# Optimization experiments

Measured on AMD Instinct MI355X. Metric: run time of the kernel, lower is better.

## Reference

```python
import math
import jax, jax.numpy as jnp
import numpy as np

B, S, H = 2, 2048, 1024
NH = 16
HD = H // NH            # 64
ROT = int(HD * 0.25)    # 16
QKV_SLOTS = 1024
PROJ_SLOTS = 1024
FFN_SLOTS = 4096
EPS = 1e-5


def gelu_l2_norm(x, axis=-1):
    # F.gelu (exact erf) then L2-normalize and rescale by sqrt(dim)
    g = jax.nn.gelu(x, approximate=False)
    n = jnp.linalg.norm(g, ord=2, axis=axis, keepdims=True)
    return g / n * math.sqrt(g.shape[axis])


def layer_norm(x, w, b):
    mu = jnp.mean(x, axis=-1, keepdims=True)
    var = jnp.mean(jnp.square(x - mu), axis=-1, keepdims=True)
    return (x - mu) * jax.lax.rsqrt(var + EPS) * w + b


def pattention(x, key_tok, val_tok):
    # [.., in] @ [slots, in]^T -> [.., slots]; NOTE: scale MULTIPLIES (as in source)
    aw = jnp.einsum('bsh,ph->bsp', x, key_tok) * math.sqrt(x.shape[-1])
    aw = gelu_l2_norm(aw, axis=-1)
    return jnp.einsum('bsp,pd->bsd', aw, val_tok)


def rotary_cos_sin(seq_len, rot_dim, base=10000.0):
    inv_freq = 1.0 / (base ** (jnp.arange(0, rot_dim, 2, dtype=jnp.float32) / rot_dim))
    t = jnp.arange(seq_len, dtype=jnp.float32)
    freqs = jnp.einsum('s,d->sd', t, inv_freq)           # [S, rot/2]
    emb = jnp.concatenate([freqs, freqs], axis=-1)       # [S, rot]
    return jnp.cos(emb), jnp.sin(emb)


def rotate_half(x):
    x1, x2 = jnp.split(x, 2, axis=-1)
    return jnp.concatenate([-x2, x1], axis=-1)


def setup_inputs() -> dict:
    key = jax.random.key(0)
    ks = jax.random.split(key, 12)
    p = lambda k, shape: jax.random.normal(k, shape, dtype=jnp.float32) * 0.02
    return {
        'x': jax.random.normal(ks[0], (B, S, H), dtype=jnp.float32),
        'ln1_w': jnp.ones((H,), jnp.float32), 'ln1_b': jnp.zeros((H,), jnp.float32),
        'ln2_w': jnp.ones((H,), jnp.float32), 'ln2_b': jnp.zeros((H,), jnp.float32),
        'q_key': p(ks[1], (QKV_SLOTS, H)), 'q_val': p(ks[2], (QKV_SLOTS, H)),
        'k_key': p(ks[3], (QKV_SLOTS, H)), 'k_val': p(ks[4], (QKV_SLOTS, H)),
        'v_key': p(ks[5], (QKV_SLOTS, H)), 'v_val': p(ks[6], (QKV_SLOTS, H)),
        'proj_key': p(ks[7], (PROJ_SLOTS, H)), 'proj_val': p(ks[8], (PROJ_SLOTS, H)),
        'ffn_key': p(ks[9], (FFN_SLOTS, H)), 'ffn_val': p(ks[10], (FFN_SLOTS, H)),
    }


def reference(x, ln1_w, ln1_b, ln2_w, ln2_b, q_key, q_val, k_key, k_val,
              v_key, v_val, proj_key, proj_val, ffn_key, ffn_val):
    residual = x
    xn = layer_norm(x, ln1_w, ln1_b)
    q = pattention(xn, q_key, q_val).reshape(B, S, NH, HD)
    k = pattention(xn, k_key, k_val).reshape(B, S, NH, HD)
    v = pattention(xn, v_key, v_val).reshape(B, S, NH, HD)

    cos, sin = rotary_cos_sin(S, ROT)          # [S, ROT]
    cos = cos[None, :, None, :]
    sin = sin[None, :, None, :]
    q_rot, q_pass = q[..., :ROT], q[..., ROT:]
    k_rot, k_pass = k[..., :ROT], k[..., ROT:]
    q_rot = q_rot * cos + rotate_half(q_rot) * sin
    k_rot = k_rot * cos + rotate_half(k_rot) * sin
    q = jnp.concatenate([q_rot, q_pass], axis=-1).transpose(0, 2, 1, 3)  # [B,NH,S,HD]
    k = jnp.concatenate([k_rot, k_pass], axis=-1).transpose(0, 2, 1, 3)
    v = v.transpose(0, 2, 1, 3)

    scale = math.sqrt(HD)
    causal = jnp.triu(jnp.ones((S, S), dtype=bool), k=1)
    attn_mask = jnp.where(causal, jnp.float32(-10000.0), jnp.float32(0.0))
    aw = jnp.einsum('bhqd,bhkd->bhqk', q, k) / scale + attn_mask
    aw = gelu_l2_norm(aw, axis=-1)
    o = jnp.einsum('bhqk,bhkd->bhqd', aw, v)
    o = o.transpose(0, 2, 1, 3).reshape(B, S, H)

    x = residual + pattention(o, proj_key, proj_val)
    residual = x
    x = residual + pattention(layer_norm(x, ln2_w, ln2_b), ffn_key, ffn_val)
    return x
```

## Files before the change

kernel.cpp:

```cpp
#include <hip/hip_runtime.h>

typedef __bf16 bf16x8 __attribute__((ext_vector_type(8)));
typedef float f32x4 __attribute__((ext_vector_type(4)));
typedef unsigned short u16;

__device__ __forceinline__ float b2f(u16 u) {
  union { unsigned int i; float f; } v; v.i = ((unsigned int)u) << 16; return v.f;
}
__device__ __forceinline__ u16 f2b(float f) {
  union { float f; unsigned int i; } v; v.f = f;
  unsigned int x = v.i;
  x += 0x7fffu + ((x >> 16) & 1u);
  return (u16)(x >> 16);
}
__device__ __forceinline__ float gelu_f(float x) {
  float x2 = x * x;
  float p = x * (1.5957691216f + 0.0713548162f * x2);
  float e = __expf(p);
  float r = __builtin_amdgcn_rcpf(1.0f + e);
  return x - x * r;
}
__device__ __forceinline__ void async16(const u16* g, u16* l) {
  __builtin_amdgcn_global_load_lds(
      (const __attribute__((address_space(1))) void*)g,
      (__attribute__((address_space(3))) void*)l, 16, 0, 0);
}
__device__ __forceinline__ void swz(int& bn, int& bm, int& bz) {
  int gx = (int)gridDim.x, gy = (int)gridDim.y;
  int flat = (int)(blockIdx.x + gridDim.x * (blockIdx.y + gridDim.y * blockIdx.z));
  int seq = flat >> 3;
  int nbm = gy >> 3;
  bm = (flat & 7) * nbm + seq % nbm;
  int rest = seq / nbm;
  bn = rest % gx;
  bz = rest / gx;
}

union U4 { uint4 u; u16 s[8]; };

__global__ __launch_bounds__(256) void prep_kernel(
    const float* __restrict__ qk, const float* __restrict__ kk,
    const float* __restrict__ vk, const float* __restrict__ pk,
    const float* __restrict__ fk, u16* __restrict__ w, float* __restrict__ ssqz,
    const float* __restrict__ qv, const float* __restrict__ kv,
    const float* __restrict__ vv, const float* __restrict__ pv,
    const float* __restrict__ fv, u16* __restrict__ valsT, u16* __restrict__ fvT,
    const float* __restrict__ x, const float* __restrict__ lnw,
    const float* __restrict__ lnb, u16* __restrict__ xn) {
  __shared__ float t[32][33];
  int id = (int)blockIdx.x;
  int tid = threadIdx.x;
  if (id < 9216) {
    int z = id >> 10;
    int i = (id & 1023) * 256 + tid;
    if (z == 8) {
      if (i < 20480) ssqz[i] = 0.f;
      return;
    }
    const float* in = (z == 0) ? qk : (z == 1) ? kk : (z == 2) ? vk : (z == 3) ? pk
                      : fk + (size_t)(z - 4) * 1048576;
    u16* o = w + (size_t)z * 1048576;
    float4 f = ((const float4*)in)[i];
    ushort4 s;
    s.x = f2b(f.x); s.y = f2b(f.y); s.z = f2b(f.z); s.w = f2b(f.w);
    ((ushort4*)o)[i] = s;
  } else if (id < 17408) {
    int rid = id - 9216;
    int bc = rid & 31, br = (rid >> 5) & 31, z = rid >> 10;
    const float* in; u16* o; int Rout, rowoff;
    if (z < 4) {
      in = (z == 0) ? qv : (z == 1) ? kv : (z == 2) ? vv : pv;
      o = valsT + (size_t)z * 1048576; Rout = 1024; rowoff = 0;
    } else {
      in = fv + (size_t)(z - 4) * 1048576;
      o = fvT; Rout = 4096; rowoff = (z - 4) * 1024;
    }
    int r = tid >> 5, cc = tid & 31;
    #pragma unroll
    for (int i = 0; i < 4; ++i)
      t[r + i * 8][cc] = in[(size_t)(br * 32 + r + i * 8) * 1024 + bc * 32 + cc];
    __syncthreads();
    #pragma unroll
    for (int i = 0; i < 4; ++i)
      o[(size_t)(bc * 32 + r + i * 8) * Rout + rowoff + br * 32 + cc] = f2b(t[cc][r + i * 8]);
  } else {
    int wv = tid >> 6, lane = tid & 63;
    int row = (id - 17408) * 4 + wv;
    const float* xr = x + (size_t)row * 1024;
    float4 v[4];
    float s = 0.f, s2 = 0.f;
    #pragma unroll
    for (int i = 0; i < 4; ++i) {
      v[i] = ((const float4*)xr)[lane + 64 * i];
      s += v[i].x + v[i].y + v[i].z + v[i].w;
      s2 += v[i].x * v[i].x + v[i].y * v[i].y + v[i].z * v[i].z + v[i].w * v[i].w;
    }
    #pragma unroll
    for (int m = 1; m < 64; m <<= 1) { s += __shfl_xor(s, m); s2 += __shfl_xor(s2, m); }
    float mu = s * (1.0f / 1024.0f);
    float inv = rsqrtf(s2 * (1.0f / 1024.0f) - mu * mu + 1e-5f);
    u16* orow = xn + (size_t)row * 1024;
    #pragma unroll
    for (int i = 0; i < 4; ++i) {
      int c = (lane + 64 * i) * 4;
      ushort4 o;
      o.x = f2b((v[i].x - mu) * inv * lnw[c]     + lnb[c]);
      o.y = f2b((v[i].y - mu) * inv * lnw[c + 1] + lnb[c + 1]);
      o.z = f2b((v[i].z - mu) * inv * lnw[c + 2] + lnb[c + 2]);
      o.w = f2b((v[i].w - mu) * inv * lnw[c + 3] + lnb[c + 3]);
      ((ushort4*)orow)[lane + 64 * i] = o;
    }
  }
}

__global__ __launch_bounds__(256) void ln_kernel(const float* __restrict__ x,
    const float* __restrict__ w, const float* __restrict__ b, u16* __restrict__ out) {
  int wv = threadIdx.x >> 6, lane = threadIdx.x & 63;
  int row = blockIdx.x * 4 + wv;
  const float* xr = x + (size_t)row * 1024;
  float4 v[4];
  float s = 0.f, s2 = 0.f;
  #pragma unroll
  for (int i = 0; i < 4; ++i) {
    v[i] = ((const float4*)xr)[lane + 64 * i];
    s += v[i].x + v[i].y + v[i].z + v[i].w;
    s2 += v[i].x * v[i].x + v[i].y * v[i].y + v[i].z * v[i].z + v[i].w * v[i].w;
  }
  #pragma unroll
  for (int m = 1; m < 64; m <<= 1) { s += __shfl_xor(s, m); s2 += __shfl_xor(s2, m); }
  float mu = s * (1.0f / 1024.0f);
  float inv = rsqrtf(s2 * (1.0f / 1024.0f) - mu * mu + 1e-5f);
  u16* orow = out + (size_t)row * 1024;
  #pragma unroll
  for (int i = 0; i < 4; ++i) {
    int c = (lane + 64 * i) * 4;
    ushort4 o;
    o.x = f2b((v[i].x - mu) * inv * w[c]     + b[c]);
    o.y = f2b((v[i].y - mu) * inv * w[c + 1] + b[c + 1]);
    o.z = f2b((v[i].z - mu) * inv * w[c + 2] + b[c + 2]);
    o.w = f2b((v[i].w - mu) * inv * w[c + 3] + b[c + 3]);
    ((ushort4*)orow)[lane + 64 * i] = o;
  }
}


template <int TM>
__global__ __launch_bounds__(256) void gemm_key(
    const u16* __restrict__ A, size_t sAz,
    const u16* __restrict__ B, size_t sBz,
    u16* __restrict__ C, size_t sCz,
    float* __restrict__ ssqb, size_t sSz,
    int N, int K, float alpha) {
  constexpr int AI = TM / 32;
  constexpr int G = TM / 64 + 2;
  __shared__ __align__(16) u16 As[3][TM * 32];
  __shared__ __align__(16) u16 Bs[3][128 * 32];
  int bn, bm, bz;
  swz(bn, bm, bz);
  const u16* Ab = A + (size_t)bz * sAz + (size_t)bm * TM * K;
  const u16* Bb = B + (size_t)bz * sBz + (size_t)bn * 128 * K;
  int tid = threadIdx.x, lane = tid & 63, wv = tid >> 6;
  int quad = lane >> 4, l16 = lane & 15;
  int lr = lane >> 2;
  int lcs = ((lane & 3) ^ ((lane >> 3) & 3)) * 8;
  int rq = quad ^ ((l16 >> 1) & 3);
  int wm = wv >> 1, wn = wv & 1;
  int RB = wm * (TM / 2), CB = wn * 64;
  auto STAGE = [&](int k0, int buf) {
    #pragma unroll
    for (int t = 0; t < TM / 64; ++t) {
      int ia = wv * (TM / 64) + t;
      async16(Ab + (size_t)(ia * 16 + lr) * K + k0 + lcs, &As[buf][ia * 512]);
    }
    #pragma unroll
    for (int t = 0; t < 2; ++t) {
      int ib = wv * 2 + t;
      async16(Bb + (size_t)(ib * 16 + lr) * K + k0 + lcs, &Bs[buf][ib * 512]);
    }
  };
  f32x4 zero = {0.f, 0.f, 0.f, 0.f};
  f32x4 acc[AI][4];
  #pragma unroll
  for (int i = 0; i < AI; ++i)
    #pragma unroll
    for (int j = 0; j < 4; ++j) acc[i][j] = zero;
  int NT = K >> 5;
  STAGE(0, 0);
  STAGE(32, 1);
  int cur = 0;
  for (int t = 0; t < NT; ++t) {
    if (t + 1 < NT) asm volatile("s_waitcnt vmcnt(%0)" :: "i"(G) : "memory");
    else            asm volatile("s_waitcnt vmcnt(0)" ::: "memory");
    __builtin_amdgcn_s_barrier();
    __builtin_amdgcn_sched_barrier(0);
    bf16x8 af[AI], bf[4];
    #pragma unroll
    for (int i = 0; i < AI; ++i)
      af[i] = *(const bf16x8*)&As[cur][(RB + i * 16 + l16) * 32 + rq * 8];
    #pragma unroll
    for (int j = 0; j < 4; ++j)
      bf[j] = *(const bf16x8*)&Bs[cur][(CB + j * 16 + l16) * 32 + rq * 8];
    if (t + 2 < NT) {
      int nb = cur + 2; if (nb >= 3) nb -= 3;
      STAGE((t + 2) * 32, nb);
    }
    #pragma unroll
    for (int i = 0; i < AI; ++i)
      #pragma unroll
      for (int j = 0; j < 4; ++j)
        acc[i][j] = __builtin_amdgcn_mfma_f32_16x16x32_bf16(af[i], bf[j], acc[i][j], 0, 0, 0);
    cur = (cur == 2) ? 0 : cur + 1;
  }
  #pragma unroll
  for (int i = 0; i < AI; ++i) {
    int rbase = bm * TM + RB + i * 16 + quad * 4;
    float srow[4] = {0.f, 0.f, 0.f, 0.f};
    #pragma unroll
    for (int j = 0; j < 4; ++j) {
      int c = bn * 128 + CB + j * 16 + l16;
      #pragma unroll
      for (int reg = 0; reg < 4; ++reg) {
        float g = gelu_f(acc[i][j][reg] * alpha);
        srow[reg] += g * g;
        C[(size_t)bz * sCz + (size_t)(rbase + reg) * N + c] = f2b(g);
      }
    }
    #pragma unroll
    for (int reg = 0; reg < 4; ++reg) {
      float s = srow[reg];
      s += __shfl_xor(s, 1); s += __shfl_xor(s, 2);
      s += __shfl_xor(s, 4); s += __shfl_xor(s, 8);
      if (l16 == 0) atomicAdd(&ssqb[bz * sSz + rbase + reg], s);
    }
  }
}

__global__ __launch_bounds__(256, 2) void gemm_fkey(
    const u16* __restrict__ A,
    const u16* __restrict__ B,
    u16* __restrict__ C,
    float* __restrict__ ssqb,
    int N, int K, float alpha) {
  __shared__ __align__(16) u16 As[2][128 * 32];
  __shared__ __align__(16) u16 Bs[3][256 * 32];
  int bn, bm, bz;
  swz(bn, bm, bz);
  const u16* Ab = A + (size_t)bm * 128 * K;
  const u16* Bb = B + (size_t)bn * 256 * K;
  int tid = threadIdx.x, lane = tid & 63, wv = tid >> 6;
  int quad = lane >> 4, l16 = lane & 15;
  int lr = lane >> 2;
  int lcs = ((lane & 3) ^ ((lane >> 3) & 3)) * 8;
  int rq = quad ^ ((l16 >> 1) & 3);
  int wm = wv >> 1, wn = wv & 1;
  int RB = wm * 64, CB = wn * 128;
  auto STAGE_A = [&](int k0, int buf) {
    #pragma unroll
    for (int t = 0; t < 2; ++t) {
      int ia = wv * 2 + t;
      async16(Ab + (size_t)(ia * 16 + lr) * K + k0 + lcs, &As[buf][ia * 512]);
    }
  };
  auto STAGE_B = [&](int k0, int buf) {
    #pragma unroll
    for (int t = 0; t < 4; ++t) {
      int ib = wv * 4 + t;
      async16(Bb + (size_t)(ib * 16 + lr) * K + k0 + lcs, &Bs[buf][ib * 512]);
    }
  };
  f32x4 zero = {0.f, 0.f, 0.f, 0.f};
  f32x4 acc[4][8];
  #pragma unroll
  for (int i = 0; i < 4; ++i)
    #pragma unroll
    for (int j = 0; j < 8; ++j) acc[i][j] = zero;
  int NT = K >> 5;
  STAGE_A(0, 0);
  STAGE_B(0, 0);
  STAGE_B(32, 1);
  int cb = 0;
  for (int t = 0; t < NT; ++t) {
    if (t + 1 < NT) asm volatile("s_waitcnt vmcnt(4)" ::: "memory");
    else            asm volatile("s_waitcnt vmcnt(0)" ::: "memory");
    __builtin_amdgcn_s_barrier();
    __builtin_amdgcn_sched_barrier(0);
    bf16x8 af[4], bf[8];
    #pragma unroll
    for (int i = 0; i < 4; ++i)
      af[i] = *(const bf16x8*)&As[t & 1][(RB + i * 16 + l16) * 32 + rq * 8];
    #pragma unroll
    for (int j = 0; j < 8; ++j)
      bf[j] = *(const bf16x8*)&Bs[cb][(CB + j * 16 + l16) * 32 + rq * 8];
    if (t + 1 < NT) STAGE_A((t + 1) * 32, (t + 1) & 1);
    if (t + 2 < NT) {
      int nb = cb + 2; if (nb >= 3) nb -= 3;
      STAGE_B((t + 2) * 32, nb);
    }
    #pragma unroll
    for (int i = 0; i < 4; ++i)
      #pragma unroll
      for (int j = 0; j < 8; ++j)
        acc[i][j] = __builtin_amdgcn_mfma_f32_16x16x32_bf16(af[i], bf[j], acc[i][j], 0, 0, 0);
    cb = (cb == 2) ? 0 : cb + 1;
  }
  #pragma unroll
  for (int i = 0; i < 4; ++i) {
    int rbase = bm * 128 + RB + i * 16 + quad * 4;
    float srow[4] = {0.f, 0.f, 0.f, 0.f};
    #pragma unroll
    for (int j = 0; j < 8; ++j) {
      int c = bn * 256 + CB + j * 16 + l16;
      #pragma unroll
      for (int reg = 0; reg < 4; ++reg) {
        float g = gelu_f(acc[i][j][reg] * alpha);
        srow[reg] += g * g;
        C[(size_t)(rbase + reg) * N + c] = f2b(g);
      }
    }
    #pragma unroll
    for (int reg = 0; reg < 4; ++reg) {
      float s = srow[reg];
      s += __shfl_xor(s, 1); s += __shfl_xor(s, 2);
      s += __shfl_xor(s, 4); s += __shfl_xor(s, 8);
      if (l16 == 0) atomicAdd(&ssqb[rbase + reg], s);
    }
  }
}

template <int TM, int MODE, bool ROT>
__global__ __launch_bounds__(256) void gemm_val(
    const u16* __restrict__ A, size_t sAz,
    const u16* __restrict__ B, size_t sBz,
    void* __restrict__ C, size_t sCz,
    const float* __restrict__ ssqb, size_t sSz,
    int N, int K, int kzs, int klen, float sqrtP, const float* __restrict__ res) {
  constexpr int AI = TM / 32;
  constexpr int G = TM / 64 + 2;
  __shared__ __align__(16) u16 As[3][TM * 32];
  __shared__ __align__(16) u16 Bs[3][128 * 32];
  int bn, bm, bz;
  swz(bn, bm, bz);
  const u16* Ab = A + (size_t)bz * sAz + (size_t)bm * TM * K;
  const u16* Bb = B + (size_t)bz * sBz + (size_t)bn * 128 * K;
  int tid = threadIdx.x, lane = tid & 63, wv = tid >> 6;
  int quad = lane >> 4, l16 = lane & 15;
  int lr = lane >> 2;
  int lcs = ((lane & 3) ^ ((lane >> 3) & 3)) * 8;
  int rq = quad ^ ((l16 >> 1) & 3);
  int wm = wv >> 1, wn = wv & 1;
  int RB = wm * (TM / 2), CB = wn * 64;
  int kb0 = bz * kzs;
  auto STAGE = [&](int k0, int buf) {
    #pragma unroll
    for (int t = 0; t < TM / 64; ++t) {
      int ia = wv * (TM / 64) + t;
      async16(Ab + (size_t)(ia * 16 + lr) * K + kb0 + k0 + lcs, &As[buf][ia * 512]);
    }
    #pragma unroll
    for (int t = 0; t < 2; ++t) {
      int ib = wv * 2 + t;
      async16(Bb + (size_t)(ib * 16 + lr) * K + kb0 + k0 + lcs, &Bs[buf][ib * 512]);
    }
  };
  f32x4 zero = {0.f, 0.f, 0.f, 0.f};
  f32x4 acc[AI][4];
  #pragma unroll
  for (int i = 0; i < AI; ++i)
    #pragma unroll
    for (int j = 0; j < 4; ++j) acc[i][j] = zero;
  int NT = klen >> 5;
  STAGE(0, 0);
  STAGE(32, 1);
  int cur = 0;
  for (int t = 0; t < NT; ++t) {
    if (t + 1 < NT) asm volatile("s_waitcnt vmcnt(%0)" :: "i"(G) : "memory");
    else            asm volatile("s_waitcnt vmcnt(0)" ::: "memory");
    __builtin_amdgcn_s_barrier();
    __builtin_amdgcn_sched_barrier(0);
    bf16x8 af[AI], bf[4];
    #pragma unroll
    for (int i = 0; i < AI; ++i)
      af[i] = *(const bf16x8*)&As[cur][(RB + i * 16 + l16) * 32 + rq * 8];
    #pragma unroll
    for (int j = 0; j < 4; ++j)
      bf[j] = *(const bf16x8*)&Bs[cur][(CB + j * 16 + l16) * 32 + rq * 8];
    if (t + 2 < NT) {
      int nb = cur + 2; if (nb >= 3) nb -= 3;
      STAGE((t + 2) * 32, nb);
    }
    #pragma unroll
    for (int i = 0; i < AI; ++i)
      #pragma unroll
      for (int j = 0; j < 4; ++j)
        acc[i][j] = __builtin_amdgcn_mfma_f32_16x16x32_bf16(af[i], bf[j], acc[i][j], 0, 0, 0);
    cur = (cur == 2) ? 0 : cur + 1;
  }
  #pragma unroll
  for (int i = 0; i < AI; ++i) {
    int rbase = bm * TM + RB + i * 16 + quad * 4;
    float sc[4];
    if (MODE < 2) {
      #pragma unroll
      for (int reg = 0; reg < 4; ++reg)
        sc[reg] = sqrtP * rsqrtf(ssqb[bz * sSz + rbase + reg]);
    }
    #pragma unroll
    for (int j = 0; j < 4; ++j) {
      int c = bn * 128 + CB + j * 16 + l16;
      #pragma unroll
      for (int reg = 0; reg < 4; ++reg) {
        float v = acc[i][j][reg];
        size_t idx = (size_t)(rbase + reg) * N + c;
        if (MODE == 0) {
          float vs = v * sc[reg];
          if (ROT && j == 0) {
            float prt = __shfl_xor(vs, 8);
            if (bz < 2) {
              int seq = (rbase + reg) & 2047;
              float fr = exp2f((float)(l16 & 7) * -1.66096404744368f);
              float ang = (float)seq * fr;
              float c_ = __cosf(ang), s_ = __sinf(ang);
              vs = (l16 < 8) ? (vs * c_ - prt * s_) : (vs * c_ + prt * s_);
            }
          }
          ((u16*)C)[(size_t)bz * sCz + idx] = f2b(vs);
        } else if (MODE == 1) {
          ((float*)C)[idx] = v * sc[reg] + res[idx];
        } else {
          ((float*)C)[(size_t)bz * sCz + idx] = v;
        }
      }
    }
  }
}

__global__ __launch_bounds__(256) void vt_kernel(const u16* __restrict__ vb,
                                                 u16* __restrict__ vT) {
  __shared__ __align__(16) u16 T[64][72];
  int st = blockIdx.x, bh = blockIdx.y;
  int b = bh >> 4, h = bh & 15;
  int tid = threadIdx.x;
  #pragma unroll
  for (int i = 0; i < 2; ++i) {
    int l = tid + 256 * i;
    int s = l >> 3, dc = l & 7;
    *(uint4*)&T[s][dc * 8] =
        *(const uint4*)(vb + (size_t)(b * 2048 + st * 64 + s) * 1024 + h * 64 + dc * 8);
  }
  __syncthreads();
  #pragma unroll
  for (int i = 0; i < 2; ++i) {
    int l = tid + 256 * i;
    int d = l >> 3, scid = l & 7;
    int blk = (scid >> 2) * 32;
    int qq = (scid & 3) * 4;
    U4 u;
    #pragma unroll
    for (int j = 0; j < 8; ++j)
      u.s[j] = T[blk + (j >> 2) * 16 + qq + (j & 3)][d];
    *(uint4*)(vT + ((size_t)bh * 64 + d) * 2048 + st * 64 + scid * 8) = u.u;
  }
}

__global__ __launch_bounds__(256) void attn_kernel(
    const u16* __restrict__ qb, const u16* __restrict__ kb,
    const u16* __restrict__ vT, u16* __restrict__ ob) {
  __shared__ __align__(16) u16 Qs[64 * 64];
  __shared__ __align__(16) u16 Ks[2][64 * 64];
  __shared__ __align__(16) u16 Vts[2][64 * 64];
  int bh = blockIdx.x;
  int qt = 31 - (int)blockIdx.y;
  int b = bh >> 4, h = bh & 15;
  const u16* qp = qb + (size_t)b * 2048 * 1024 + h * 64;
  const u16* kp = kb + (size_t)b * 2048 * 1024 + h * 64;
  const u16* vp = vT + (size_t)bh * 64 * 2048;
  int tid = threadIdx.x, lane = tid & 63, wv = tid >> 6;
  int quad = lane >> 4, l16 = lane & 15;
  int lr8 = lane >> 3;
  int lc8s = ((lane & 7) ^ lr8) * 8;
  int rx = (l16 & 7) << 3;
  int MR = wv * 16;
  int nkt = qt + 1;
  #pragma unroll
  for (int t = 0; t < 2; ++t) {
    int idx = wv * 2 + t;
    async16(qp + (size_t)(qt * 64 + idx * 8 + lr8) * 1024 + lc8s, &Qs[idx * 512]);
    async16(kp + (size_t)(idx * 8 + lr8) * 1024 + lc8s, &Ks[0][idx * 512]);
    async16(vp + (size_t)(idx * 8 + lr8) * 2048 + lc8s, &Vts[0][idx * 512]);
  }
  f32x4 zero = {0.f, 0.f, 0.f, 0.f};
  f32x4 oacc[4];
  #pragma unroll
  for (int dn = 0; dn < 4; ++dn) oacc[dn] = zero;
  float ssql = 0.f;
  bf16x8 bq0 = {}, bq1 = {};
  for (int kt = 0, cur = 0; kt < nkt; ++kt, cur ^= 1) {
    __syncthreads();
    if (kt == 0) {
      bq0 = *(const bf16x8*)&Qs[((MR + l16) * 64 + quad * 8) ^ rx];
      bq1 = *(const bf16x8*)&Qs[((MR + l16) * 64 + 32 + quad * 8) ^ rx];
    }
    if (kt + 1 < nkt) {
      #pragma unroll
      for (int t = 0; t < 2; ++t) {
        int idx = wv * 2 + t;
        async16(kp + (size_t)((kt + 1) * 64 + idx * 8 + lr8) * 1024 + lc8s, &Ks[cur ^ 1][idx * 512]);
        async16(vp + (size_t)(idx * 8 + lr8) * 2048 + (kt + 1) * 64 + lc8s, &Vts[cur ^ 1][idx * 512]);
      }
    }
    bool dg = (kt == qt);
    #pragma unroll
    for (int kc = 0; kc < 2; ++kc) {
      bf16x8 pf;
      #pragma unroll
      for (int snh = 0; snh < 2; ++snh) {
        int sn = kc * 2 + snh;
        bf16x8 ak0 = *(const bf16x8*)&Ks[cur][((sn * 16 + l16) * 64 + quad * 8) ^ rx];
        bf16x8 ak1 = *(const bf16x8*)&Ks[cur][((sn * 16 + l16) * 64 + 32 + quad * 8) ^ rx];
        f32x4 st = zero;
        st = __builtin_amdgcn_mfma_f32_16x16x32_bf16(ak0, bq0, st, 0, 0, 0);
        st = __builtin_amdgcn_mfma_f32_16x16x32_bf16(ak1, bq1, st, 0, 0, 0);
        #pragma unroll
        for (int r = 0; r < 4; ++r) {
          float gl = gelu_f(st[r] * 0.125f);
          if (dg && (sn * 16 + quad * 4 + r > MR + l16)) gl = 0.f;
          ssql += gl * gl;
          pf[snh * 4 + r] = (__bf16)gl;
        }
      }
      #pragma unroll
      for (int dn = 0; dn < 4; ++dn) {
        bf16x8 bv = *(const bf16x8*)&Vts[cur][((dn * 16 + l16) * 64 + kc * 32 + quad * 8) ^ rx];
        oacc[dn] = __builtin_amdgcn_mfma_f32_16x16x32_bf16(pf, bv, oacc[dn], 0, 0, 0);
      }
    }
  }
  ssql += __shfl_xor(ssql, 16);
  ssql += __shfl_xor(ssql, 32);
  float sc = 45.254834f * rsqrtf(ssql);
  #pragma unroll
  for (int dn = 0; dn < 4; ++dn)
    #pragma unroll
    for (int r = 0; r < 4; ++r) {
      float scr = __shfl(sc, quad * 4 + r);
      int row = qt * 64 + MR + quad * 4 + r;
      int col = h * 64 + dn * 16 + l16;
      ob[(size_t)(b * 2048 + row) * 1024 + col] = f2b(oacc[dn][r] * scr);
    }
}

__global__ __launch_bounds__(256) void fin_kernel(
    const float* __restrict__ p0, const float* __restrict__ p1,
    const float* __restrict__ x1, const float* __restrict__ ssqf,
    float* __restrict__ out) {
  int row = blockIdx.x, t = threadIdx.x;
  float s = 64.0f * rsqrtf(ssqf[row]);
  size_t base = (size_t)row * 1024 + t * 4;
  float4 a = *(const float4*)(p0 + base);
  float4 b = *(const float4*)(p1 + base);
  float4 r = *(const float4*)(x1 + base);
  float4 o;
  o.x = r.x + s * (a.x + b.x); o.y = r.y + s * (a.y + b.y);
  o.z = r.z + s * (a.z + b.z); o.w = r.w + s * (a.w + b.w);
  *(float4*)(out + base) = o;
}

extern "C" void kernel_launch(void* const* d_in, const int* in_sizes, int n_in,
                              void* d_out, int out_size, void* d_ws, size_t ws_size,
                              hipStream_t stream) {
  const float* x    = (const float*)d_in[0];
  const float* ln1w = (const float*)d_in[1];
  const float* ln1b = (const float*)d_in[2];
  const float* ln2w = (const float*)d_in[3];
  const float* ln2b = (const float*)d_in[4];
  const float* qk   = (const float*)d_in[5];
  const float* qv   = (const float*)d_in[6];
  const float* kk   = (const float*)d_in[7];
  const float* kv   = (const float*)d_in[8];
  const float* vk   = (const float*)d_in[9];
  const float* vv   = (const float*)d_in[10];
  const float* pk   = (const float*)d_in[11];
  const float* pv   = (const float*)d_in[12];
  const float* fk   = (const float*)d_in[13];
  const float* fv   = (const float*)d_in[14];
  float* out = (float*)d_out;

  const size_t M1 = 1048576;
  u16* w = (u16*)d_ws;
  u16* wkeys  = w;
  u16* wpk    = w + 3 * M1;
  u16* wfk    = w + 4 * M1;
  u16* wvalsT = w + 8 * M1;
  u16* wpvT   = w + 11 * M1;
  u16* wfvT   = w + 12 * M1;
  u16* xn     = w + 16 * M1;
  u16* gq     = w + 20 * M1;
  u16* ob     = w + 20 * M1;
  u16* vT     = w + 24 * M1;
  u16* gp     = w + 28 * M1;
  u16* gf     = w + 20 * M1;
  u16* qb     = w + 36 * M1;
  u16* kb     = w + 40 * M1;
  u16* vb     = w + 44 * M1;
  float* ssq_qkv  = (float*)(w + 48 * M1);
  float* ssq_proj = ssq_qkv + 12288;
  float* ssq_ffn  = ssq_qkv + 16384;
  float* x1 = (float*)(w + 52 * M1);
  float* p0 = (float*)w;
  float* p1 = (float*)(w + 36 * M1);

  dim3 blk(256);
  prep_kernel<<<18432, blk, 0, stream>>>(
      qk, kk, vk, pk, fk, w, ssq_qkv,
      qv, kv, vv, pv, fv, wvalsT, wfvT,
      x, ln1w, ln1b, xn);

  gemm_key<128><<<dim3(8, 32, 3), blk, 0, stream>>>(
      xn, 0, wkeys, M1, gq, 4 * M1, ssq_qkv, 4096, 1024, 1024, 32.0f);
  gemm_val<128, 0, true><<<dim3(8, 32, 3), blk, 0, stream>>>(
      gq, 4 * M1, wvalsT, M1, qb, 4 * M1, ssq_qkv, 4096, 1024, 1024, 0, 1024, 32.0f, nullptr);

  vt_kernel<<<dim3(32, 32), blk, 0, stream>>>(vb, vT);
  attn_kernel<<<dim3(32, 32), blk, 0, stream>>>(qb, kb, vT, ob);

  gemm_key<64><<<dim3(8, 64, 1), blk, 0, stream>>>(
      ob, 0, wpk, 0, gp, 0, ssq_proj, 0, 1024, 1024, 32.0f);
  gemm_val<64, 1, false><<<dim3(8, 64, 1), blk, 0, stream>>>(
      gp, 0, wpvT, 0, x1, 0, ssq_proj, 0, 1024, 1024, 0, 1024, 32.0f, x);

  ln_kernel<<<1024, blk, 0, stream>>>(x1, ln2w, ln2b, xn);
  gemm_fkey<<<dim3(16, 32, 1), blk, 0, stream>>>(
      xn, wfk, gf, ssq_ffn, 4096, 1024, 32.0f);
  gemm_val<128, 2, false><<<dim3(8, 32, 2), blk, 0, stream>>>(
      gf, 0, wfvT, 0, p0, 18 * M1, ssq_ffn, 0, 1024, 4096, 2048, 2048, 0.0f, nullptr);
  fin_kernel<<<4096, blk, 0, stream>>>(p0, p1, x1, ssq_ffn, out);
}
```

Baseline: 407.9 us.

## Split long causal attention rows into two KV halves with a combine kernel

The causal attention grid is rebalanced: query tiles 17..31 are each split into two blocks covering halves of the key range, and the two blocks write unnormalized partial outputs and partial sum-of-squares to scratch. A new combine kernel adds the partials, applies the L2 rescale and writes bf16 output. This aims to cut the tail from the longest query tiles on a 32x32 grid. It costs an extra launch and fp32 scratch traffic. GELU also switches to exp2 with pre-scaled coefficients.

Result: no change. 401.5 us (-1.6%).

```diff
diff --git a/kernel.cpp b/kernel.cpp
--- a/kernel.cpp
+++ b/kernel.cpp
@@ -15,8 +15,8 @@
 }
 __device__ __forceinline__ float gelu_f(float x) {
   float x2 = x * x;
-  float p = x * (1.5957691216f + 0.0713548162f * x2);
-  float e = __expf(p);
+  float p = x * (2.3022083f + 0.1029434f * x2);
+  float e = __builtin_amdgcn_exp2f(p);
   float r = __builtin_amdgcn_rcpf(1.0f + e);
   return x - x * r;
 }
@@ -142,7 +142,6 @@
     ((ushort4*)orow)[lane + 64 * i] = o;
   }
 }
-
 
 template <int TM>
 __global__ __launch_bounds__(256) void gemm_key(
@@ -463,16 +462,26 @@
 }
 
 __global__ __launch_bounds__(256) void attn_kernel(
-    const u16* __restrict__ qb, const u16* __restrict__ kb,
-    const u16* __restrict__ vT, u16* __restrict__ ob) {
+    const u16* __restrict__ qb, const u16* __restrict__ kbp,
+    const u16* __restrict__ vT, u16* __restrict__ ob,
+    float* __restrict__ pP, float* __restrict__ ssqP) {
   __shared__ __align__(16) u16 Qs[64 * 64];
   __shared__ __align__(16) u16 Ks[2][64 * 64];
   __shared__ __align__(16) u16 Vts[2][64 * 64];
   int bh = blockIdx.x;
-  int qt = 31 - (int)blockIdx.y;
-  int b = bh >> 4, h = bh & 15;
-  const u16* qp = qb + (size_t)b * 2048 * 1024 + h * 64;
-  const u16* kp = kb + (size_t)b * 2048 * 1024 + h * 64;
+  int y = (int)blockIdx.y;
+  int qt, kb, ke, half = 0;
+  bool part = false;
+  if (y == 0) { qt = 16; kb = 0; ke = 17; }
+  else if (y <= 30) {
+    int s = y - 1;
+    qt = 31 - (s >> 1); half = s & 1; part = true;
+    int n = qt + 1, h = (n + 1) >> 1;
+    kb = half ? h : 0; ke = half ? n : h;
+  } else { qt = 46 - y; kb = 0; ke = qt + 1; }
+  int b = bh >> 4, h16 = bh & 15;
+  const u16* qp = qb + (size_t)b * 2048 * 1024 + h16 * 64;
+  const u16* kp = kbp + (size_t)b * 2048 * 1024 + h16 * 64;
   const u16* vp = vT + (size_t)bh * 64 * 2048;
   int tid = threadIdx.x, lane = tid & 63, wv = tid >> 6;
   int quad = lane >> 4, l16 = lane & 15;
@@ -480,13 +489,12 @@
   int lc8s = ((lane & 7) ^ lr8) * 8;
   int rx = (l16 & 7) << 3;
   int MR = wv * 16;
-  int nkt = qt + 1;
   #pragma unroll
   for (int t = 0; t < 2; ++t) {
     int idx = wv * 2 + t;
     async16(qp + (size_t)(qt * 64 + idx * 8 + lr8) * 1024 + lc8s, &Qs[idx * 512]);
-    async16(kp + (size_t)(idx * 8 + lr8) * 1024 + lc8s, &Ks[0][idx * 512]);
-    async16(vp + (size_t)(idx * 8 + lr8) * 2048 + lc8s, &Vts[0][idx * 512]);
+    async16(kp + (size_t)(kb * 64 + idx * 8 + lr8) * 1024 + lc8s, &Ks[0][idx * 512]);
+    async16(vp + (size_t)(idx * 8 + lr8) * 2048 + kb * 64 + lc8s, &Vts[0][idx * 512]);
   }
   f32x4 zero = {0.f, 0.f, 0.f, 0.f};
   f32x4 oacc[4];
@@ -494,13 +502,13 @@
   for (int dn = 0; dn < 4; ++dn) oacc[dn] = zero;
   float ssql = 0.f;
   bf16x8 bq0 = {}, bq1 = {};
-  for (int kt = 0, cur = 0; kt < nkt; ++kt, cur ^= 1) {
+  for (int kt = kb, cur = 0; kt < ke; ++kt, cur ^= 1) {
     __syncthreads();
-    if (kt == 0) {
+    if (kt == kb) {
       bq0 = *(const bf16x8*)&Qs[((MR + l16) * 64 + quad * 8) ^ rx];
       bq1 = *(const bf16x8*)&Qs[((MR + l16) * 64 + 32 + quad * 8) ^ rx];
     }
-    if (kt + 1 < nkt) {
+    if (kt + 1 < ke) {
       #pragma unroll
       for (int t = 0; t < 2; ++t) {
         int idx = wv * 2 + t;
@@ -537,16 +545,50 @@
   }
   ssql += __shfl_xor(ssql, 16);
   ssql += __shfl_xor(ssql, 32);
-  float sc = 45.254834f * rsqrtf(ssql);
-  #pragma unroll
-  for (int dn = 0; dn < 4; ++dn)
-    #pragma unroll
-    for (int r = 0; r < 4; ++r) {
-      float scr = __shfl(sc, quad * 4 + r);
-      int row = qt * 64 + MR + quad * 4 + r;
-      int col = h * 64 + dn * 16 + l16;
-      ob[(size_t)(b * 2048 + row) * 1024 + col] = f2b(oacc[dn][r] * scr);
-    }
+  if (!part) {
+    float sc = 45.254834f * rsqrtf(ssql);
+    #pragma unroll
+    for (int dn = 0; dn < 4; ++dn)
+      #pragma unroll
+      for (int r = 0; r < 4; ++r) {
+        float scr = __shfl(sc, quad * 4 + r);
+        int row = qt * 64 + MR + quad * 4 + r;
+        int col = h16 * 64 + dn * 16 + l16;
+        ob[(size_t)(b * 2048 + row) * 1024 + col] = f2b(oacc[dn][r] * scr);
+      }
+  } else {
+    int sp = ((qt - 17) * 32 + bh) * 2 + half;
+    if (lane < 16) ssqP[sp * 64 + MR + l16] = ssql;
+    float* po = pP + (size_t)sp * 4096;
+    #pragma unroll
+    for (int dn = 0; dn < 4; ++dn)
+      #pragma unroll
+      for (int r = 0; r < 4; ++r)
+        po[(MR + quad * 4 + r) * 64 + dn * 16 + l16] = oacc[dn][r];
+  }
+}
+
+__global__ __launch_bounds__(256) void acmb_kernel(
+    const float* __restrict__ pP, const float* __restrict__ ssqP,
+    u16* __restrict__ ob) {
+  int s = blockIdx.x;
+  int qt = 17 + (s >> 5), bh = s & 31;
+  int b = bh >> 4, h = bh & 15;
+  const float* p0 = pP + (size_t)(2 * s) * 4096;
+  const float* p1 = p0 + 4096;
+  int tid = threadIdx.x;
+  int row = tid >> 2, c0 = (tid & 3) * 16;
+  float sc = 45.254834f * rsqrtf(ssqP[(2 * s) * 64 + row] + ssqP[(2 * s + 1) * 64 + row]);
+  u16* orow = ob + (size_t)(b * 2048 + qt * 64 + row) * 1024 + h * 64 + c0;
+  #pragma unroll
+  for (int i = 0; i < 16; i += 4) {
+    float4 a = *(const float4*)(p0 + row * 64 + c0 + i);
+    float4 c = *(const float4*)(p1 + row * 64 + c0 + i);
+    ushort4 o;
+    o.x = f2b((a.x + c.x) * sc); o.y = f2b((a.y + c.y) * sc);
+    o.z = f2b((a.z + c.z) * sc); o.w = f2b((a.w + c.w) * sc);
+    *(ushort4*)(orow + i) = o;
+  }
 }
 
 __global__ __launch_bounds__(256) void fin_kernel(
@@ -608,6 +650,8 @@
   float* x1 = (float*)(w + 52 * M1);
   float* p0 = (float*)w;
   float* p1 = (float*)(w + 36 * M1);
+  float* pP   = (float*)(w + 28 * M1);
+  float* ssqP = (float*)(w + 52 * M1);
 
   dim3 blk(256);
   prep_kernel<<<18432, blk, 0, stream>>>(
@@ -621,7 +665,8 @@
       gq, 4 * M1, wvalsT, M1, qb, 4 * M1, ssq_qkv, 4096, 1024, 1024, 0, 1024, 32.0f, nullptr);
 
   vt_kernel<<<dim3(32, 32), blk, 0, stream>>>(vb, vT);
-  attn_kernel<<<dim3(32, 32), blk, 0, stream>>>(qb, kb, vT, ob);
+  attn_kernel<<<dim3(32, 47), blk, 0, stream>>>(qb, kb, vT, ob, pP, ssqP);
+  acmb_kernel<<<480, blk, 0, stream>>>(pP, ssqP, ob);
 
   gemm_key<64><<<dim3(8, 64, 1), blk, 0, stream>>>(
       ob, 0, wpk, 0, gp, 0, ssq_proj, 0, 1024, 1024, 32.0f);
```
